# Optimization experiments

Hardware: AMD Instinct MI355X
Metric: run time of the kernel (lower is better)

## Reference

```python
import jax, jax.numpy as jnp
import numpy as np

B, S, H, NH = 16, 512, 768, 12
HD = H // NH


def setup_inputs() -> dict:
    key = jax.random.key(0)
    ks = jax.random.split(key, 8)
    w = 0.02
    return {
        "x": jax.random.normal(ks[0], (B, S, H), jnp.float32),
        "key_padding_mask": jnp.zeros((B, S), jnp.bool_),
        "in_proj_w": jax.random.normal(ks[1], (3 * H, H), jnp.float32) * w,
        "in_proj_b": jnp.zeros((3 * H,), jnp.float32),
        "out_proj_w": jax.random.normal(ks[2], (H, H), jnp.float32) * w,
        "out_proj_b": jnp.zeros((H,), jnp.float32),
        "w1": jax.random.normal(ks[3], (4 * H, H), jnp.float32) * w,
        "b1": jnp.zeros((4 * H,), jnp.float32),
        "w2": jax.random.normal(ks[4], (H, 4 * H), jnp.float32) * w,
        "b2": jnp.zeros((H,), jnp.float32),
        "ln1_g": jnp.ones((H,), jnp.float32),
        "ln1_b": jnp.zeros((H,), jnp.float32),
        "ln2_g": jnp.ones((H,), jnp.float32),
        "ln2_b": jnp.zeros((H,), jnp.float32),
    }


def _layernorm(x, g, b, eps=1e-5):
    m = jnp.mean(x, axis=-1, keepdims=True)
    v = jnp.var(x, axis=-1, keepdims=True)
    return (x - m) / jnp.sqrt(v + eps) * g + b


def reference(x, key_padding_mask, in_proj_w, in_proj_b, out_proj_w, out_proj_b,
              w1, b1, w2, b2, ln1_g, ln1_b, ln2_g, ln2_b):
    b, s, h = x.shape
    # --- nn.MultiheadAttention (batch_first, need_weights, per-head weights) ---
    qkv = x @ in_proj_w.T + in_proj_b                      # [B,S,3H]
    q, k, v = jnp.split(qkv, 3, axis=-1)
    q = q.reshape(b, s, NH, HD).transpose(0, 2, 1, 3)      # [B,NH,S,HD]
    k = k.reshape(b, s, NH, HD).transpose(0, 2, 1, 3)
    v = v.reshape(b, s, NH, HD).transpose(0, 2, 1, 3)
    scale = 1.0 / np.sqrt(HD).astype(np.float32)
    scores = jnp.einsum('bhqd,bhkd->bhqk', q * scale, k)   # [B,NH,S,S]
    scores = jnp.where(key_padding_mask[:, None, None, :], -jnp.inf, scores)
    attn_weights = jax.nn.softmax(scores, axis=-1)         # returned per-head
    attn_out = jnp.einsum('bhqk,bhkd->bhqd', attn_weights, v)
    attn_out = attn_out.transpose(0, 2, 1, 3).reshape(b, s, h)
    attn_out = attn_out @ out_proj_w.T + out_proj_b
    # --- residual + LN, FFN + residual + LN (dropout is identity in eval) ---
    x = _layernorm(x + attn_out, ln1_g, ln1_b)
    ffn = jax.nn.gelu(x @ w1.T + b1, approximate=False) @ w2.T + b2
    x = _layernorm(x + ffn, ln2_g, ln2_b)
    return x, attn_weights
```

## Files before the change

kernel.cpp:

```cpp
#include <hip/hip_runtime.h>
#include <hip/hip_bf16.h>
#include <math.h>

typedef __bf16 bf16;
typedef __attribute__((ext_vector_type(8))) __bf16 bf16x8;
typedef __attribute__((ext_vector_type(4))) __bf16 bf16x4;
typedef __attribute__((ext_vector_type(4))) float f32x4;

#define B_  16
#define S_  512
#define H_  768
#define NH_ 12
#define HD_ 64
#define A_  (B_*S_)

__device__ __forceinline__ void gload_lds16(const void* g, void* l) {
  __builtin_amdgcn_global_load_lds((const __attribute__((address_space(1))) void*)g,
                                   (__attribute__((address_space(3))) void*)l, 16, 0, 0);
}

#define GBM 128
#define GBN 192
#define GBK 64
#define SLOT_E 20480

template<int EPI>
__global__ __launch_bounds__(512, 2) void k_gemm(
    const bf16* __restrict__ Amat, const bf16* __restrict__ Bt,
    const float* __restrict__ bias, const float* __restrict__ res,
    float* __restrict__ outF, bf16* __restrict__ outB,
    bf16* __restrict__ outQ, bf16* __restrict__ outK, bf16* __restrict__ outVT,
    int M, int N, int K)
{
  __shared__ __align__(16) bf16 LDS[3*SLOT_E];
  const int tid = threadIdx.x;
  const int w = tid >> 6, l = tid & 63;
  const int lr = l & 15, hi = l >> 4;
  const int wm = w >> 2, wn = w & 3;

  const int nbx = N / GBN;
  const int cpx = gridDim.x >> 3;
  const int sw  = (blockIdx.x & 7) * cpx + (blockIdx.x >> 3);
  const int by = sw / nbx, bx = sw - by * nbx;
  const int row0 = by * GBM, col0 = bx * GBN;
  const int NT = K / GBK;

  auto stage = [&](int t, int u) {
    bf16* slot = LDS + (t % 3) * SLOT_E;
    if (u < 2) {
      const int fc = u*512 + tid;
      const int r = fc >> 3, s = fc & 7;
      const int gs = s ^ (r & 7);
      gload_lds16(Amat + (size_t)(row0 + r)*K + t*GBK + gs*8,
                  slot + (size_t)fc*8 - (size_t)l*8);
    } else {
      const int fc = (u-2)*512 + tid;
      const int r = fc >> 3, s = fc & 7;
      const int gs = s ^ (r & 7);
      gload_lds16(Bt + (size_t)(col0 + r)*K + t*GBK + gs*8,
                  slot + 8192 + (size_t)fc*8 - (size_t)l*8);
    }
  };

  f32x4 acc[4][3] = {};

#pragma unroll
  for (int u = 0; u < 5; ++u) stage(0, u);
#pragma unroll
  for (int u = 0; u < 5; ++u) stage(1, u);
  asm volatile("s_waitcnt vmcnt(5)" ::: "memory");
  __builtin_amdgcn_s_barrier();

  for (int t = 0; t < NT; ++t) {
    const bf16* slot = LDS + (t % 3) * SLOT_E;
    const bool pre = (t + 2 < NT);

    bf16x8 af[4], bfr[3];
#pragma unroll
    for (int m = 0; m < 4; ++m) {
      const int r = wm*64 + m*16 + lr;
      af[m] = *(const bf16x8*)(slot + r*64 + (hi ^ (r & 7))*8);
    }
#pragma unroll
    for (int n = 0; n < 3; ++n) {
      const int r = wn*48 + n*16 + lr;
      bfr[n] = *(const bf16x8*)(slot + 8192 + r*64 + (hi ^ (r & 7))*8);
    }
    if (pre) { stage(t+2, 0); stage(t+2, 1); stage(t+2, 2); }
    __builtin_amdgcn_s_barrier();
    asm volatile("s_waitcnt lgkmcnt(0)" ::: "memory");
    __builtin_amdgcn_sched_barrier(0);
    __builtin_amdgcn_s_setprio(1);
#pragma unroll
    for (int m = 0; m < 4; ++m)
#pragma unroll
      for (int n = 0; n < 3; ++n)
        acc[m][n] = __builtin_amdgcn_mfma_f32_16x16x32_bf16(af[m], bfr[n], acc[m][n], 0, 0, 0);
    __builtin_amdgcn_s_setprio(0);
    __builtin_amdgcn_s_barrier();

#pragma unroll
    for (int m = 0; m < 4; ++m) {
      const int r = wm*64 + m*16 + lr;
      af[m] = *(const bf16x8*)(slot + r*64 + ((4 + hi) ^ (r & 7))*8);
    }
#pragma unroll
    for (int n = 0; n < 3; ++n) {
      const int r = wn*48 + n*16 + lr;
      bfr[n] = *(const bf16x8*)(slot + 8192 + r*64 + ((4 + hi) ^ (r & 7))*8);
    }
    if (pre) { stage(t+2, 3); stage(t+2, 4); }
    __builtin_amdgcn_s_barrier();
    asm volatile("s_waitcnt lgkmcnt(0)" ::: "memory");
    __builtin_amdgcn_sched_barrier(0);
    __builtin_amdgcn_s_setprio(1);
#pragma unroll
    for (int m = 0; m < 4; ++m)
#pragma unroll
      for (int n = 0; n < 3; ++n)
        acc[m][n] = __builtin_amdgcn_mfma_f32_16x16x32_bf16(af[m], bfr[n], acc[m][n], 0, 0, 0);
    __builtin_amdgcn_s_setprio(0);

    if (t < NT - 1) {
      if (pre) asm volatile("s_waitcnt vmcnt(5)" ::: "memory");
      else     asm volatile("s_waitcnt vmcnt(0)" ::: "memory");
      __builtin_amdgcn_s_barrier();
    }
  }

#pragma unroll
  for (int m = 0; m < 4; ++m) {
#pragma unroll
    for (int n = 0; n < 3; ++n) {
#pragma unroll
      for (int i = 0; i < 4; ++i) {
        const int row = row0 + wm*64 + m*16 + hi*4 + i;
        const int col = col0 + wn*48 + n*16 + lr;
        float v = acc[m][n][i] + bias[col];
        if constexpr (EPI == 1) {
          v += res[(size_t)row*N + col];
          outF[(size_t)row*N + col] = v;
        } else if constexpr (EPI == 2) {
          v = 0.5f * v * (1.0f + erff(v * 0.7071067811865475f));
          outB[(size_t)row*N + col] = (bf16)v;
        } else {
          const int b = row >> 9, s = row & 511;
          const int which = col / H_;
          const int hcol = col - which * H_;
          const int h = hcol >> 6, d = hcol & 63;
          const size_t bh = (size_t)b * NH_ + h;
          if (which == 0)      outQ[(bh*S_ + s)*HD_ + d] = (bf16)v;
          else if (which == 1) outK[(bh*S_ + s)*HD_ + d] = (bf16)v;
          else                 outVT[(bh*HD_ + d)*S_ + s] = (bf16)v;
        }
      }
    }
  }
}

__global__ __launch_bounds__(256) void k_attn_fused(
    const bf16* __restrict__ Qm, const bf16* __restrict__ Km, const bf16* __restrict__ VT,
    const unsigned char* __restrict__ mask, float* __restrict__ P, bf16* __restrict__ AO)
{
  __shared__ __align__(16) bf16 KVs[512*64];
  __shared__ __align__(16) bf16 Qs[64*64];
  const int tid = threadIdx.x, w = tid >> 6, l = tid & 63;
  const int lr = l & 15, hi = l >> 4;
  const int bh = blockIdx.x, qt = blockIdx.y;
  const int b = bh / NH_, h = bh - b * NH_;
  const int swz = (lr & 7) << 4;

  const bf16* Kg = Km + (size_t)bh * S_ * HD_;
  const bf16* Qg = Qm + (size_t)bh * S_ * HD_ + (size_t)qt * 64 * HD_;
#pragma unroll
  for (int rnd = 0; rnd < 16; ++rnd) {
    const int c = rnd*256 + tid;
    const int row = c >> 3, col16 = (c & 7) ^ (row & 7);
    gload_lds16(Kg + row*HD_ + col16*8, KVs + (rnd*4 + w)*512);
  }
#pragma unroll
  for (int rnd = 0; rnd < 2; ++rnd) {
    const int c = rnd*256 + tid;
    const int row = c >> 3, col16 = (c & 7) ^ (row & 7);
    gload_lds16(Qg + row*HD_ + col16*8, Qs + (rnd*4 + w)*512);
  }
  __syncthreads();

  const char* qrow = (const char*)(Qs + (w*16 + lr)*64);
  bf16x8 qf0 = *(const bf16x8*)(qrow + ((hi*16) ^ swz));
  bf16x8 qf1 = *(const bf16x8*)(qrow + ((64 + hi*16) ^ swz));
  f32x4 acc[32];
#pragma unroll
  for (int ct = 0; ct < 32; ++ct) acc[ct] = f32x4{0.f,0.f,0.f,0.f};
#pragma unroll
  for (int ct = 0; ct < 32; ++ct) {
    const char* kb = (const char*)(KVs + (ct*16 + lr)*64);
    bf16x8 a0 = *(const bf16x8*)(kb + ((hi*16) ^ swz));
    bf16x8 a1 = *(const bf16x8*)(kb + ((64 + hi*16) ^ swz));
    acc[ct] = __builtin_amdgcn_mfma_f32_16x16x32_bf16(a0, qf0, acc[ct], 0, 0, 0);
    acc[ct] = __builtin_amdgcn_mfma_f32_16x16x32_bf16(a1, qf1, acc[ct], 0, 0, 0);
  }
  __syncthreads();

  const bf16* Vg = VT + (size_t)bh * HD_ * S_;
#pragma unroll
  for (int rnd = 0; rnd < 16; ++rnd) {
    const int c = rnd*256 + tid;
    const int row = c >> 6, col16 = (c & 63) ^ (row & 7);
    gload_lds16(Vg + row*S_ + col16*8, KVs + (rnd*4 + w)*512);
  }

  const unsigned char* mrow = mask + b * S_;
  float mx = -1e30f;
#pragma unroll
  for (int ct = 0; ct < 32; ++ct) {
    const unsigned mk4 = *(const unsigned*)(mrow + ct*16 + hi*4);
#pragma unroll
    for (int i = 0; i < 4; ++i) {
      float v = acc[ct][i] * 0.125f;
      if ((mk4 >> (8*i)) & 0xff) v = -1e30f;
      acc[ct][i] = v;
      mx = fmaxf(mx, v);
    }
  }
  mx = fmaxf(mx, __shfl_xor(mx, 16));
  mx = fmaxf(mx, __shfl_xor(mx, 32));
  float sum = 0.f;
#pragma unroll
  for (int ct = 0; ct < 32; ++ct)
#pragma unroll
    for (int i = 0; i < 4; ++i) { float e = __expf(acc[ct][i] - mx); acc[ct][i] = e; sum += e; }
  sum += __shfl_xor(sum, 16);
  sum += __shfl_xor(sum, 32);
  const float inv = 1.f / sum;

  float* prow = P + ((size_t)bh*S_ + (size_t)qt*64 + w*16 + lr) * S_;
#pragma unroll
  for (int ct = 0; ct < 32; ++ct) {
#pragma unroll
    for (int i = 0; i < 4; ++i) acc[ct][i] *= inv;
    *(f32x4*)(prow + ct*16 + hi*4) = acc[ct];
  }
  __syncthreads();

  f32x4 o[4] = {};
#pragma unroll
  for (int c = 0; c < 16; ++c) {
    bf16x8 pa;
#pragma unroll
    for (int i = 0; i < 4; ++i) { pa[i] = (bf16)acc[2*c][i]; pa[4+i] = (bf16)acc[2*c+1][i]; }
    const int cb0 = (64*c + 8*hi) ^ swz;
    const int cb1 = (64*c + 32 + 8*hi) ^ swz;
#pragma unroll
    for (int nt = 0; nt < 4; ++nt) {
      const char* vb = (const char*)(KVs + (nt*16 + lr)*512);
      bf16x4 v0 = *(const bf16x4*)(vb + cb0);
      bf16x4 v1 = *(const bf16x4*)(vb + cb1);
      bf16x8 vf = {v0[0],v0[1],v0[2],v0[3], v1[0],v1[1],v1[2],v1[3]};
      o[nt] = __builtin_amdgcn_mfma_f32_16x16x32_bf16(pa, vf, o[nt], 0, 0, 0);
    }
  }

  bf16* aorow = AO + ((size_t)(b*S_ + qt*64 + w*16))*H_ + h*HD_;
#pragma unroll
  for (int nt = 0; nt < 4; ++nt)
#pragma unroll
    for (int i = 0; i < 4; ++i)
      aorow[(size_t)(hi*4 + i)*H_ + nt*16 + lr] = (bf16)o[nt][i];
}

__global__ __launch_bounds__(256) void k_layernorm(
    const float* __restrict__ X, const float* __restrict__ g, const float* __restrict__ bta,
    float* __restrict__ outF, bf16* __restrict__ outB)
{
  const int row = blockIdx.x;
  const int tid = threadIdx.x;
  const float* x = X + (size_t)row * H_;
  float v[3]; float s = 0.f, ss = 0.f;
#pragma unroll
  for (int j = 0; j < 3; ++j) { v[j] = x[tid + j*256]; s += v[j]; ss += v[j]*v[j]; }
#pragma unroll
  for (int d = 1; d < 64; d <<= 1) { s += __shfl_xor(s, d); ss += __shfl_xor(ss, d); }
  __shared__ float red[8];
  const int w = tid >> 6, l = tid & 63;
  if (l == 0) { red[w] = s; red[4 + w] = ss; }
  __syncthreads();
  s  = red[0] + red[1] + red[2] + red[3];
  ss = red[4] + red[5] + red[6] + red[7];
  const float mean = s * (1.f / H_);
  const float var  = ss * (1.f / H_) - mean * mean;
  const float inv  = rsqrtf(var + 1e-5f);
#pragma unroll
  for (int j = 0; j < 3; ++j) {
    const int c = tid + j*256;
    const float y = (v[j] - mean) * inv * g[c] + bta[c];
    if (outF) outF[(size_t)row*H_ + c] = y;
    if (outB) outB[(size_t)row*H_ + c] = (bf16)y;
  }
}

__global__ void k_f32_bf16(const float* __restrict__ in, bf16* __restrict__ out, int n) {
  const int i = (blockIdx.x * 256 + threadIdx.x) * 4;
  if (i < n) {
    const float4 vv = *(const float4*)(in + i);
    bf16x4 o; o[0]=(bf16)vv.x; o[1]=(bf16)vv.y; o[2]=(bf16)vv.z; o[3]=(bf16)vv.w;
    *(bf16x4*)(out + i) = o;
  }
}

extern "C" void kernel_launch(void* const* d_in, const int* in_sizes, int n_in,
                              void* d_out, int out_size, void* d_ws, size_t ws_size,
                              hipStream_t stream) {
  const float* x      = (const float*)d_in[0];
  const unsigned char* mask = (const unsigned char*)d_in[1];
  const float* w_qkv  = (const float*)d_in[2];
  const float* b_qkv  = (const float*)d_in[3];
  const float* w_out  = (const float*)d_in[4];
  const float* b_out  = (const float*)d_in[5];
  const float* w1     = (const float*)d_in[6];
  const float* b1     = (const float*)d_in[7];
  const float* w2     = (const float*)d_in[8];
  const float* b2     = (const float*)d_in[9];
  const float* ln1g   = (const float*)d_in[10];
  const float* ln1b   = (const float*)d_in[11];
  const float* ln2g   = (const float*)d_in[12];
  const float* ln2b   = (const float*)d_in[13];

  float* xout = (float*)d_out;
  float* P    = xout + (size_t)A_ * H_;

  char* ws = (char*)d_ws;
  size_t off = 0;
  auto alloc = [&](size_t bytes) { char* p = ws + off; off += (bytes + 255) & ~255ull; return p; };

  bf16* xb   = (bf16*)alloc((size_t)A_*H_*2);
  bf16* wqkv = (bf16*)alloc((size_t)3*H_*H_*2);
  bf16* wo   = (bf16*)alloc((size_t)H_*H_*2);
  bf16* w1b  = (bf16*)alloc((size_t)4*H_*H_*2);
  bf16* w2b  = (bf16*)alloc((size_t)4*H_*H_*2);
  char* qreg = alloc((size_t)A_*H_*2*4);
  bf16* q  = (bf16*)qreg;
  bf16* kb = q  + (size_t)A_*H_;
  bf16* vt = kb + (size_t)A_*H_;
  bf16* ao = vt + (size_t)A_*H_;
  bf16* hbuf = q;
  float* y1  = (float*)alloc((size_t)A_*H_*4);
  float* x1f = (float*)alloc((size_t)A_*H_*4);
  bf16*  x1b = (bf16*)alloc((size_t)A_*H_*2);

  k_f32_bf16<<<A_*H_/1024,      256, 0, stream>>>(x,     xb,   A_*H_);
  k_f32_bf16<<<3*H_*H_/1024,    256, 0, stream>>>(w_qkv, wqkv, 3*H_*H_);
  k_f32_bf16<<<H_*H_/1024,      256, 0, stream>>>(w_out, wo,   H_*H_);
  k_f32_bf16<<<4*H_*H_/1024,    256, 0, stream>>>(w1,    w1b,  4*H_*H_);
  k_f32_bf16<<<4*H_*H_/1024,    256, 0, stream>>>(w2,    w2b,  4*H_*H_);

  k_gemm<0><<<(A_/GBM)*(3*H_/GBN), 512, 0, stream>>>(xb, wqkv, b_qkv, nullptr,
      nullptr, nullptr, q, kb, vt, A_, 3*H_, H_);
  k_attn_fused<<<dim3(B_*NH_, S_/64), 256, 0, stream>>>(q, kb, vt, mask, P, ao);
  k_gemm<1><<<(A_/GBM)*(H_/GBN), 512, 0, stream>>>(ao, wo, b_out, x,
      y1, nullptr, nullptr, nullptr, nullptr, A_, H_, H_);
  k_layernorm<<<A_, 256, 0, stream>>>(y1, ln1g, ln1b, x1f, x1b);
  k_gemm<2><<<(A_/GBM)*(4*H_/GBN), 512, 0, stream>>>(x1b, w1b, b1, nullptr,
      nullptr, hbuf, nullptr, nullptr, nullptr, A_, 4*H_, H_);
  k_gemm<1><<<(A_/GBM)*(H_/GBN), 512, 0, stream>>>(hbuf, w2b, b2, x1f,
      y1, nullptr, nullptr, nullptr, nullptr, A_, H_, 4*H_);
  k_layernorm<<<A_, 256, 0, stream>>>(y1, ln2g, ln2b, xout, nullptr);
}
```

Measured before the change: 354.7 us.

## Template GEMM tile width, fuse weight conversions, use bf16 residual for FFN2

Makes the GEMM N-tile a template parameter and uses 256-wide tiles for the QKV and FFN1 GEMMs. It merges the five fp32-to-bf16 conversion launches into one kernel. It drops the fp32 copy of the LN1 output and feeds the bf16 copy as the FFN2 residual, which saves a full fp32 write and read. The larger LDS footprint of the wider tile may cut blocks per CU, and the bf16 residual slightly reduces precision.

```diff
diff --git a/kernel.cpp b/kernel.cpp
--- a/kernel.cpp
+++ b/kernel.cpp
@@ -19,31 +19,31 @@
                                    (__attribute__((address_space(3))) void*)l, 16, 0, 0);
 }
 
-#define GBM 128
-#define GBN 192
-#define GBK 64
-#define SLOT_E 20480
-
-template<int EPI>
+template<int EPI, int BN_>
 __global__ __launch_bounds__(512, 2) void k_gemm(
     const bf16* __restrict__ Amat, const bf16* __restrict__ Bt,
-    const float* __restrict__ bias, const float* __restrict__ res,
+    const float* __restrict__ bias, const float* __restrict__ resF,
+    const bf16* __restrict__ resB,
     float* __restrict__ outF, bf16* __restrict__ outB,
     bf16* __restrict__ outQ, bf16* __restrict__ outK, bf16* __restrict__ outVT,
     int M, int N, int K)
 {
-  __shared__ __align__(16) bf16 LDS[3*SLOT_E];
+  constexpr int NFRAG  = BN_ / 64;
+  constexpr int UNITS  = 2 + NFRAG;
+  constexpr int SLOT_E = 8192 + BN_ * 64;
+  constexpr int WN     = BN_ / 4;
+  __shared__ __align__(16) bf16 LDS[3 * SLOT_E];
   const int tid = threadIdx.x;
   const int w = tid >> 6, l = tid & 63;
   const int lr = l & 15, hi = l >> 4;
   const int wm = w >> 2, wn = w & 3;
 
-  const int nbx = N / GBN;
+  const int nbx = N / BN_;
   const int cpx = gridDim.x >> 3;
   const int sw  = (blockIdx.x & 7) * cpx + (blockIdx.x >> 3);
   const int by = sw / nbx, bx = sw - by * nbx;
-  const int row0 = by * GBM, col0 = bx * GBN;
-  const int NT = K / GBK;
+  const int row0 = by * 128, col0 = bx * BN_;
+  const int NT = K / 64;
 
   auto stage = [&](int t, int u) {
     bf16* slot = LDS + (t % 3) * SLOT_E;
@@ -51,42 +51,46 @@
       const int fc = u*512 + tid;
       const int r = fc >> 3, s = fc & 7;
       const int gs = s ^ (r & 7);
-      gload_lds16(Amat + (size_t)(row0 + r)*K + t*GBK + gs*8,
+      gload_lds16(Amat + (size_t)(row0 + r)*K + t*64 + gs*8,
                   slot + (size_t)fc*8 - (size_t)l*8);
     } else {
       const int fc = (u-2)*512 + tid;
       const int r = fc >> 3, s = fc & 7;
       const int gs = s ^ (r & 7);
-      gload_lds16(Bt + (size_t)(col0 + r)*K + t*GBK + gs*8,
+      gload_lds16(Bt + (size_t)(col0 + r)*K + t*64 + gs*8,
                   slot + 8192 + (size_t)fc*8 - (size_t)l*8);
     }
   };
 
-  f32x4 acc[4][3] = {};
-
-#pragma unroll
-  for (int u = 0; u < 5; ++u) stage(0, u);
-#pragma unroll
-  for (int u = 0; u < 5; ++u) stage(1, u);
-  asm volatile("s_waitcnt vmcnt(5)" ::: "memory");
+  f32x4 acc[4][NFRAG] = {};
+
+#pragma unroll
+  for (int u = 0; u < UNITS; ++u) stage(0, u);
+#pragma unroll
+  for (int u = 0; u < UNITS; ++u) stage(1, u);
+  if constexpr (UNITS == 5) asm volatile("s_waitcnt vmcnt(5)" ::: "memory");
+  else                      asm volatile("s_waitcnt vmcnt(6)" ::: "memory");
   __builtin_amdgcn_s_barrier();
 
   for (int t = 0; t < NT; ++t) {
     const bf16* slot = LDS + (t % 3) * SLOT_E;
     const bool pre = (t + 2 < NT);
 
-    bf16x8 af[4], bfr[3];
+    bf16x8 af[4], bfr[NFRAG];
 #pragma unroll
     for (int m = 0; m < 4; ++m) {
       const int r = wm*64 + m*16 + lr;
       af[m] = *(const bf16x8*)(slot + r*64 + (hi ^ (r & 7))*8);
     }
 #pragma unroll
-    for (int n = 0; n < 3; ++n) {
-      const int r = wn*48 + n*16 + lr;
+    for (int n = 0; n < NFRAG; ++n) {
+      const int r = wn*WN + n*16 + lr;
       bfr[n] = *(const bf16x8*)(slot + 8192 + r*64 + (hi ^ (r & 7))*8);
     }
-    if (pre) { stage(t+2, 0); stage(t+2, 1); stage(t+2, 2); }
+    if (pre) {
+      stage(t+2, 0); stage(t+2, 1); stage(t+2, 2);
+      if constexpr (UNITS == 6) stage(t+2, 3);
+    }
     __builtin_amdgcn_s_barrier();
     asm volatile("s_waitcnt lgkmcnt(0)" ::: "memory");
     __builtin_amdgcn_sched_barrier(0);
@@ -94,7 +98,7 @@
 #pragma unroll
     for (int m = 0; m < 4; ++m)
 #pragma unroll
-      for (int n = 0; n < 3; ++n)
+      for (int n = 0; n < NFRAG; ++n)
         acc[m][n] = __builtin_amdgcn_mfma_f32_16x16x32_bf16(af[m], bfr[n], acc[m][n], 0, 0, 0);
     __builtin_amdgcn_s_setprio(0);
     __builtin_amdgcn_s_barrier();
@@ -105,11 +109,14 @@
       af[m] = *(const bf16x8*)(slot + r*64 + ((4 + hi) ^ (r & 7))*8);
     }
 #pragma unroll
-    for (int n = 0; n < 3; ++n) {
-      const int r = wn*48 + n*16 + lr;
+    for (int n = 0; n < NFRAG; ++n) {
+      const int r = wn*WN + n*16 + lr;
       bfr[n] = *(const bf16x8*)(slot + 8192 + r*64 + ((4 + hi) ^ (r & 7))*8);
     }
-    if (pre) { stage(t+2, 3); stage(t+2, 4); }
+    if (pre) {
+      if constexpr (UNITS == 5) { stage(t+2, 3); stage(t+2, 4); }
+      else                      { stage(t+2, 4); stage(t+2, 5); }
+    }
     __builtin_amdgcn_s_barrier();
     asm volatile("s_waitcnt lgkmcnt(0)" ::: "memory");
     __builtin_amdgcn_sched_barrier(0);
@@ -117,13 +124,17 @@
 #pragma unroll
     for (int m = 0; m < 4; ++m)
 #pragma unroll
-      for (int n = 0; n < 3; ++n)
+      for (int n = 0; n < NFRAG; ++n)
         acc[m][n] = __builtin_amdgcn_mfma_f32_16x16x32_bf16(af[m], bfr[n], acc[m][n], 0, 0, 0);
     __builtin_amdgcn_s_setprio(0);
 
     if (t < NT - 1) {
-      if (pre) asm volatile("s_waitcnt vmcnt(5)" ::: "memory");
-      else     asm volatile("s_waitcnt vmcnt(0)" ::: "memory");
+      if (pre) {
+        if constexpr (UNITS == 5) asm volatile("s_waitcnt vmcnt(5)" ::: "memory");
+        else                      asm volatile("s_waitcnt vmcnt(6)" ::: "memory");
+      } else {
+        asm volatile("s_waitcnt vmcnt(0)" ::: "memory");
+      }
       __builtin_amdgcn_s_barrier();
     }
   }
@@ -131,18 +142,21 @@
 #pragma unroll
   for (int m = 0; m < 4; ++m) {
 #pragma unroll
-    for (int n = 0; n < 3; ++n) {
+    for (int n = 0; n < NFRAG; ++n) {
 #pragma unroll
       for (int i = 0; i < 4; ++i) {
         const int row = row0 + wm*64 + m*16 + hi*4 + i;
-        const int col = col0 + wn*48 + n*16 + lr;
+        const int col = col0 + wn*WN + n*16 + lr;
         float v = acc[m][n][i] + bias[col];
         if constexpr (EPI == 1) {
-          v += res[(size_t)row*N + col];
+          v += resF[(size_t)row*N + col];
           outF[(size_t)row*N + col] = v;
         } else if constexpr (EPI == 2) {
           v = 0.5f * v * (1.0f + erff(v * 0.7071067811865475f));
           outB[(size_t)row*N + col] = (bf16)v;
+        } else if constexpr (EPI == 3) {
+          v += (float)resB[(size_t)row*N + col];
+          outF[(size_t)row*N + col] = v;
         } else {
           const int b = row >> 9, s = row & 511;
           const int which = col / H_;
@@ -299,13 +313,29 @@
   }
 }
 
-__global__ void k_f32_bf16(const float* __restrict__ in, bf16* __restrict__ out, int n) {
-  const int i = (blockIdx.x * 256 + threadIdx.x) * 4;
-  if (i < n) {
-    const float4 vv = *(const float4*)(in + i);
-    bf16x4 o; o[0]=(bf16)vv.x; o[1]=(bf16)vv.y; o[2]=(bf16)vv.z; o[3]=(bf16)vv.w;
-    *(bf16x4*)(out + i) = o;
-  }
+#define NB0 (A_*H_/1024)
+#define NB1 (3*H_*H_/1024)
+#define NB2 (H_*H_/1024)
+#define NB3 (4*H_*H_/1024)
+#define NB4 (4*H_*H_/1024)
+__global__ void k_conv_all(
+    const float* __restrict__ s0, bf16* __restrict__ d0,
+    const float* __restrict__ s1, bf16* __restrict__ d1,
+    const float* __restrict__ s2, bf16* __restrict__ d2,
+    const float* __restrict__ s3, bf16* __restrict__ d3,
+    const float* __restrict__ s4, bf16* __restrict__ d4)
+{
+  int b = blockIdx.x;
+  const float* src; bf16* dst;
+  if      (b < NB0)                   { src = s0; dst = d0; }
+  else if ((b -= NB0) < NB1)          { src = s1; dst = d1; }
+  else if ((b -= NB1) < NB2)          { src = s2; dst = d2; }
+  else if ((b -= NB2) < NB3)          { src = s3; dst = d3; }
+  else    { b -= NB3;                   src = s4; dst = d4; }
+  const int i = (b * 256 + threadIdx.x) * 4;
+  const float4 vv = *(const float4*)(src + i);
+  bf16x4 o; o[0]=(bf16)vv.x; o[1]=(bf16)vv.y; o[2]=(bf16)vv.z; o[3]=(bf16)vv.w;
+  *(bf16x4*)(dst + i) = o;
 }
 
 extern "C" void kernel_launch(void* const* d_in, const int* in_sizes, int n_in,
@@ -345,24 +375,20 @@
   bf16* ao = vt + (size_t)A_*H_;
   bf16* hbuf = q;
   float* y1  = (float*)alloc((size_t)A_*H_*4);
-  float* x1f = (float*)alloc((size_t)A_*H_*4);
   bf16*  x1b = (bf16*)alloc((size_t)A_*H_*2);
 
-  k_f32_bf16<<<A_*H_/1024,      256, 0, stream>>>(x,     xb,   A_*H_);
-  k_f32_bf16<<<3*H_*H_/1024,    256, 0, stream>>>(w_qkv, wqkv, 3*H_*H_);
-  k_f32_bf16<<<H_*H_/1024,      256, 0, stream>>>(w_out, wo,   H_*H_);
-  k_f32_bf16<<<4*H_*H_/1024,    256, 0, stream>>>(w1,    w1b,  4*H_*H_);
-  k_f32_bf16<<<4*H_*H_/1024,    256, 0, stream>>>(w2,    w2b,  4*H_*H_);
-
-  k_gemm<0><<<(A_/GBM)*(3*H_/GBN), 512, 0, stream>>>(xb, wqkv, b_qkv, nullptr,
+  k_conv_all<<<NB0+NB1+NB2+NB3+NB4, 256, 0, stream>>>(
+      x, xb, w_qkv, wqkv, w_out, wo, w1, w1b, w2, w2b);
+
+  k_gemm<0,256><<<(A_/128)*(3*H_/256), 512, 0, stream>>>(xb, wqkv, b_qkv, nullptr, nullptr,
       nullptr, nullptr, q, kb, vt, A_, 3*H_, H_);
   k_attn_fused<<<dim3(B_*NH_, S_/64), 256, 0, stream>>>(q, kb, vt, mask, P, ao);
-  k_gemm<1><<<(A_/GBM)*(H_/GBN), 512, 0, stream>>>(ao, wo, b_out, x,
+  k_gemm<1,192><<<(A_/128)*(H_/192), 512, 0, stream>>>(ao, wo, b_out, x, nullptr,
       y1, nullptr, nullptr, nullptr, nullptr, A_, H_, H_);
-  k_layernorm<<<A_, 256, 0, stream>>>(y1, ln1g, ln1b, x1f, x1b);
-  k_gemm<2><<<(A_/GBM)*(4*H_/GBN), 512, 0, stream>>>(x1b, w1b, b1, nullptr,
+  k_layernorm<<<A_, 256, 0, stream>>>(y1, ln1g, ln1b, nullptr, x1b);
+  k_gemm<2,256><<<(A_/128)*(4*H_/256), 512, 0, stream>>>(x1b, w1b, b1, nullptr, nullptr,
       nullptr, hbuf, nullptr, nullptr, nullptr, A_, 4*H_, H_);
-  k_gemm<1><<<(A_/GBM)*(H_/GBN), 512, 0, stream>>>(hbuf, w2b, b2, x1f,
+  k_gemm<3,192><<<(A_/128)*(H_/192), 512, 0, stream>>>(hbuf, w2b, b2, nullptr, x1b,
       y1, nullptr, nullptr, nullptr, nullptr, A_, H_, 4*H_);
   k_layernorm<<<A_, 256, 0, stream>>>(y1, ln2g, ln2b, xout, nullptr);
 }
```

Measured after the change: 331.7 us. -6.5%, faster.
